# Kernel tuning notes

Measured on AMD Instinct MI355X. Metric: run time of the kernel, lower is better.

## Reference

```python
import jax, jax.numpy as jnp
import numpy as np

ALPHA, GAMMA, EPS = 0.25, 2.0, 1e-8
W_CLASS, W_BBOX, W_GIOU = 1.0, 1.0, 1.0


def box_cxcywh_to_xyxy(b):
    cx, cy, w, h = b[..., 0], b[..., 1], b[..., 2], b[..., 3]
    return jnp.stack([cx - 0.5 * w, cy - 0.5 * h, cx + 0.5 * w, cy + 0.5 * h], axis=-1)


def generalized_box_iou(a, b):
    # a: [N,4] xyxy, b: [T,4] xyxy -> [N,T]
    area_a = (a[:, 2] - a[:, 0]) * (a[:, 3] - a[:, 1])
    area_b = (b[:, 2] - b[:, 0]) * (b[:, 3] - b[:, 1])
    lt = jnp.maximum(a[:, None, :2], b[None, :, :2])
    rb = jnp.minimum(a[:, None, 2:], b[None, :, 2:])
    wh = jnp.clip(rb - lt, 0.0)
    inter = wh[..., 0] * wh[..., 1]
    union = area_a[:, None] + area_b[None, :] - inter
    iou = inter / union
    lt_c = jnp.minimum(a[:, None, :2], b[None, :, :2])
    rb_c = jnp.maximum(a[:, None, 2:], b[None, :, 2:])
    wh_c = jnp.clip(rb_c - lt_c, 0.0)
    area_c = wh_c[..., 0] * wh_c[..., 1]
    return iou - (area_c - union) / area_c


def setup_inputs() -> dict:
    key = jax.random.key(0)
    k1, k2, k3, k4 = jax.random.split(key, 4)
    bs, Q, C, T = 16, 900, 91, 1600
    return {
        "pred_logits": jax.random.normal(k1, (bs, Q, C), dtype=jnp.float32),
        "pred_boxes": jax.random.uniform(k2, (bs, Q, 4), dtype=jnp.float32),
        "tgt_labels": jax.random.randint(k3, (T,), 0, C),
        "tgt_boxes": jax.random.uniform(k4, (T, 4), dtype=jnp.float32),
    }


def reference(pred_logits, pred_boxes, tgt_labels, tgt_boxes):
    bs, num_queries = pred_logits.shape[:2]
    out_prob = jax.nn.sigmoid(pred_logits.reshape(-1, pred_logits.shape[-1]))  # [N,C]
    out_bbox = pred_boxes.reshape(-1, 4)  # [N,4]

    # sigmoid focal classification cost, gathered at target class ids
    neg = (1.0 - ALPHA) * out_prob ** GAMMA * -jnp.log(1.0 - out_prob + EPS)
    pos = ALPHA * (1.0 - out_prob) ** GAMMA * -jnp.log(out_prob + EPS)
    cost_class = pos[:, tgt_labels] - neg[:, tgt_labels]  # [N,T]

    # L1 cdist over cxcywh boxes
    cost_bbox = jnp.sum(jnp.abs(out_bbox[:, None, :] - tgt_boxes[None, :, :]), axis=-1)  # [N,T]

    # negative generalized IoU
    cost_giou = -generalized_box_iou(box_cxcywh_to_xyxy(out_bbox), box_cxcywh_to_xyxy(tgt_boxes))

    C = W_BBOX * cost_bbox + W_CLASS * cost_class + W_GIOU * cost_giou
    # [bs, num_queries, total_targets]; per-image blocks C[b, :, b*n:(b+1)*n] feed
    # the (host-side, non-differentiable) linear_sum_assignment in the original.
    return C.reshape(bs, num_queries, -1)
```

## Files before the change

### kernel.cpp

```cpp
#include <hip/hip_runtime.h>
#include <math.h>

namespace {
constexpr int BS = 16, Q = 900, CN = 91, T = 1600;
constexpr int N  = BS * Q;
constexpr float kALPHA = 0.25f;
constexpr float kEPS   = 1e-8f;

constexpr int TT = 320;
constexpr int NT = 32;

__global__ __launch_bounds__(TT) void k_cost(
    const float*  __restrict__ logits,
    const float4* __restrict__ pboxes,
    const float4* __restrict__ tboxes,
    const int*    __restrict__ tlab,
    float*        __restrict__ out)
{
    __shared__ float sK[NT * CN];

    const int tid = threadIdx.x;
    const int t0  = blockIdx.x * TT;
    const int n0  = blockIdx.y * NT;

    const float4 tb = tboxes[t0 + tid];
    const int    tl = tlab[t0 + tid];
    const float tcx = tb.x, tcy = tb.y, tw = tb.z, th = tb.w;
    const float tx0 = tcx - 0.5f * tw, ty0 = tcy - 0.5f * th;
    const float tx1 = tcx + 0.5f * tw, ty1 = tcy + 0.5f * th;
    const float tar = (tx1 - tx0) * (ty1 - ty0);

    for (int i = tid; i < NT * CN; i += TT) {
        float x  = logits[n0 * CN + i];
        float p  = 1.0f / (1.0f + expf(-x));
        float om = 1.0f - p;
        float pos = kALPHA          * om * om * (-logf(p  + kEPS));
        float neg = (1.0f - kALPHA) * p  * p  * (-logf(om + kEPS));
        sK[i] = pos - neg;
    }
    __syncthreads();

    float* outp = out + t0 + tid;

    #pragma unroll 4
    for (int i = 0; i < NT; ++i) {
        const int n = n0 + i;
        const float4 braw = pboxes[n];
        const float  cls  = sK[i * CN + tl];

        const float bx0 = braw.x - 0.5f * braw.z, by0 = braw.y - 0.5f * braw.w;
        const float bx1 = braw.x + 0.5f * braw.z, by1 = braw.y + 0.5f * braw.w;
        const float aA  = (bx1 - bx0) * (by1 - by0);

        float l1 = fabsf(braw.x - tcx) + fabsf(braw.y - tcy)
                 + fabsf(braw.z - tw ) + fabsf(braw.w - th );

        float ix0 = fmaxf(bx0, tx0), iy0 = fmaxf(by0, ty0);
        float ix1 = fminf(bx1, tx1), iy1 = fminf(by1, ty1);
        float iw  = fmaxf(ix1 - ix0, 0.0f), ih = fmaxf(iy1 - iy0, 0.0f);
        float inter = iw * ih;
        float uni   = aA + tar - inter;

        float cx0 = fminf(bx0, tx0), cy0 = fminf(by0, ty0);
        float cx1 = fmaxf(bx1, tx1), cy1 = fmaxf(by1, ty1);
        float aC  = (cx1 - cx0) * (cy1 - cy0);

        float giou_cost = 1.0f - inter * __builtin_amdgcn_rcpf(uni)
                               - uni   * __builtin_amdgcn_rcpf(aC);

        outp[n * T] = l1 + cls + giou_cost;
    }
}
}

extern "C" void kernel_launch(void* const* d_in, const int* in_sizes, int n_in,
                              void* d_out, int out_size, void* d_ws, size_t ws_size,
                              hipStream_t stream)
{
    const float*  logits = (const float*) d_in[0];
    const float4* pboxes = (const float4*)d_in[1];
    const int*    tlab   = (const int*)   d_in[2];
    const float4* tboxes = (const float4*)d_in[3];
    float*        out    = (float*)d_out;

    dim3 grid(T / TT, N / NT);
    hipLaunchKernelGGL(k_cost, grid, dim3(TT), 0, stream,
                       logits, pboxes, tboxes, tlab, out);
}
```

Baseline: 134.2 us.

## Cover full target row per block with 4-wide columns and float4 stores

Each block now owns 16 prediction rows and all 1600 targets. Each thread handles 4 consecutive targets (up to two column groups) and writes them with float4 stores. This means the logits sigmoid/focal table is computed once per row group rather than once per target tile, and wider stores cut store instruction count. The costs are more registers per thread, uneven work (some threads take two column groups and others one), and 4-way gathered LDS reads.

After: 145.3 us. 1.08x slower.

```diff
diff --git a/kernel.cpp b/kernel.cpp
--- a/kernel.cpp
+++ b/kernel.cpp
@@ -7,10 +7,11 @@
 constexpr float kALPHA = 0.25f;
 constexpr float kEPS   = 1e-8f;
 
-constexpr int TT = 320;
-constexpr int NT = 32;
+constexpr int NT   = 16;
+constexpr int BT   = 256;
+constexpr int NCOL = T / 4;
 
-__global__ __launch_bounds__(TT) void k_cost(
+__global__ __launch_bounds__(BT, 4) void k_cost(
     const float*  __restrict__ logits,
     const float4* __restrict__ pboxes,
     const float4* __restrict__ tboxes,
@@ -20,55 +21,80 @@
     __shared__ float sK[NT * CN];
 
     const int tid = threadIdx.x;
-    const int t0  = blockIdx.x * TT;
-    const int n0  = blockIdx.y * NT;
+    const int n0  = blockIdx.x * NT;
 
-    const float4 tb = tboxes[t0 + tid];
-    const int    tl = tlab[t0 + tid];
-    const float tcx = tb.x, tcy = tb.y, tw = tb.z, th = tb.w;
-    const float tx0 = tcx - 0.5f * tw, ty0 = tcy - 0.5f * th;
-    const float tx1 = tcx + 0.5f * tw, ty1 = tcy + 0.5f * th;
-    const float tar = (tx1 - tx0) * (ty1 - ty0);
-
-    for (int i = tid; i < NT * CN; i += TT) {
+    for (int i = tid; i < NT * CN; i += BT) {
         float x  = logits[n0 * CN + i];
         float p  = 1.0f / (1.0f + expf(-x));
         float om = 1.0f - p;
-        float pos = kALPHA          * om * om * (-logf(p  + kEPS));
-        float neg = (1.0f - kALPHA) * p  * p  * (-logf(om + kEPS));
-        sK[i] = pos - neg;
+        sK[i] = kALPHA          * om * om * (-logf(p  + kEPS))
+              - (1.0f - kALPHA) * p  * p  * (-logf(om + kEPS));
+    }
+
+    const int ncol_th = (tid < NCOL - BT) ? 2 : 1;
+    float tcx[2][4], tcy[2][4], tww[2][4], thh[2][4], tar[2][4];
+    int   tl [2][4];
+    #pragma unroll
+    for (int j = 0; j < 2; ++j) {
+        if (j < ncol_th) {
+            const int c = tid + j * BT;
+            const int4 lab = *reinterpret_cast<const int4*>(tlab + 4 * c);
+            tl[j][0] = lab.x; tl[j][1] = lab.y; tl[j][2] = lab.z; tl[j][3] = lab.w;
+            #pragma unroll
+            for (int k = 0; k < 4; ++k) {
+                const float4 b = tboxes[4 * c + k];
+                tcx[j][k] = b.x; tcy[j][k] = b.y; tww[j][k] = b.z; thh[j][k] = b.w;
+                const float x0 = b.x - 0.5f * b.z, y0 = b.y - 0.5f * b.w;
+                const float x1 = b.x + 0.5f * b.z, y1 = b.y + 0.5f * b.w;
+                tar[j][k] = (x1 - x0) * (y1 - y0);
+            }
+        }
     }
     __syncthreads();
-
-    float* outp = out + t0 + tid;
 
     #pragma unroll 4
     for (int i = 0; i < NT; ++i) {
         const int n = n0 + i;
         const float4 braw = pboxes[n];
-        const float  cls  = sK[i * CN + tl];
-
         const float bx0 = braw.x - 0.5f * braw.z, by0 = braw.y - 0.5f * braw.w;
         const float bx1 = braw.x + 0.5f * braw.z, by1 = braw.y + 0.5f * braw.w;
         const float aA  = (bx1 - bx0) * (by1 - by0);
+        float* orow = out + (size_t)n * T;
 
-        float l1 = fabsf(braw.x - tcx) + fabsf(braw.y - tcy)
-                 + fabsf(braw.z - tw ) + fabsf(braw.w - th );
+        #pragma unroll
+        for (int j = 0; j < 2; ++j) {
+            if (j < ncol_th) {
+                float4 r;
+                #pragma unroll
+                for (int k = 0; k < 4; ++k) {
+                    const float cx = tcx[j][k], cy = tcy[j][k];
+                    const float w  = tww[j][k], h  = thh[j][k];
+                    const float x0 = cx - 0.5f * w, y0 = cy - 0.5f * h;
+                    const float x1 = cx + 0.5f * w, y1 = cy + 0.5f * h;
 
-        float ix0 = fmaxf(bx0, tx0), iy0 = fmaxf(by0, ty0);
-        float ix1 = fminf(bx1, tx1), iy1 = fminf(by1, ty1);
-        float iw  = fmaxf(ix1 - ix0, 0.0f), ih = fmaxf(iy1 - iy0, 0.0f);
-        float inter = iw * ih;
-        float uni   = aA + tar - inter;
+                    float l1 = fabsf(braw.x - cx) + fabsf(braw.y - cy)
+                             + fabsf(braw.z - w ) + fabsf(braw.w - h );
 
-        float cx0 = fminf(bx0, tx0), cy0 = fminf(by0, ty0);
-        float cx1 = fmaxf(bx1, tx1), cy1 = fmaxf(by1, ty1);
-        float aC  = (cx1 - cx0) * (cy1 - cy0);
+                    float ix0 = fmaxf(bx0, x0), iy0 = fmaxf(by0, y0);
+                    float ix1 = fminf(bx1, x1), iy1 = fminf(by1, y1);
+                    float inter = fmaxf(ix1 - ix0, 0.0f) * fmaxf(iy1 - iy0, 0.0f);
+                    float uni   = aA + tar[j][k] - inter;
 
-        float giou_cost = 1.0f - inter * __builtin_amdgcn_rcpf(uni)
-                               - uni   * __builtin_amdgcn_rcpf(aC);
+                    float cx0 = fminf(bx0, x0), cy0 = fminf(by0, y0);
+                    float cx1 = fmaxf(bx1, x1), cy1 = fmaxf(by1, y1);
+                    float aC  = (cx1 - cx0) * (cy1 - cy0);
 
-        outp[n * T] = l1 + cls + giou_cost;
+                    const float cls = sK[i * CN + tl[j][k]];
+
+                    float v = l1 + cls + 1.0f
+                            - inter * __builtin_amdgcn_rcpf(uni)
+                            - uni   * __builtin_amdgcn_rcpf(aC);
+                    if (k == 0) r.x = v; else if (k == 1) r.y = v;
+                    else if (k == 2) r.z = v; else r.w = v;
+                }
+                *reinterpret_cast<float4*>(orow + 4 * (tid + j * BT)) = r;
+            }
+        }
     }
 }
 }
@@ -83,7 +109,6 @@
     const float4* tboxes = (const float4*)d_in[3];
     float*        out    = (float*)d_out;
 
-    dim3 grid(T / TT, N / NT);
-    hipLaunchKernelGGL(k_cost, grid, dim3(TT), 0, stream,
+    hipLaunchKernelGGL(k_cost, dim3(N / NT), dim3(BT), 0, stream,
                        logits, pboxes, tboxes, tlab, out);
 }
```
